# Performance work log

Measured on AMD Instinct MI355X. Metric: run time of the kernel, lower is better.

Reference implementation:

```python
import jax, jax.numpy as jnp
import numpy as np

N, S, C, G = 40000, 16, 96, 12
EPS = 1e-5

def ln(x, g, b):
    mu = jnp.mean(x, -1, keepdims=True)
    var = jnp.mean((x - mu) ** 2, -1, keepdims=True)
    return (x - mu) * jax.lax.rsqrt(var + EPS) * g + b

def setup_inputs() -> dict:
    key = jax.random.key(0)
    ks = jax.random.split(key, 20)
    s = 0.05
    inp = {
        'q': jax.random.normal(ks[0], (N, C), jnp.float32),
        'k': jax.random.normal(ks[1], (N, C), jnp.float32),
        'v': jax.random.normal(ks[2], (N, C), jnp.float32),
        'xyz': jax.random.normal(ks[3], (N, 3), jnp.float32),
        'reference_index': jax.random.randint(ks[4], (N, S), 0, N, jnp.int32),
        # linear_q: Linear(C,C)+LN(C)+ReLU
        'Wq': jax.random.normal(ks[5], (C, C), jnp.float32) * s,
        'bq': jnp.zeros((C,), jnp.float32),
        'gq': jnp.ones((C,), jnp.float32),
        'betaq': jnp.zeros((C,), jnp.float32),
        # linear_k
        'Wk': jax.random.normal(ks[6], (C, C), jnp.float32) * s,
        'bk': jnp.zeros((C,), jnp.float32),
        'gk': jnp.ones((C,), jnp.float32),
        'betak': jnp.zeros((C,), jnp.float32),
        # linear_v
        'Wv': jax.random.normal(ks[7], (C, C), jnp.float32) * s,
        'bv': jnp.zeros((C,), jnp.float32),
        # linear_p_bias: Linear(3,C)+LN(C)+ReLU+Linear(C,C)
        'Wp1': jax.random.normal(ks[8], (3, C), jnp.float32) * s,
        'bp1': jnp.zeros((C,), jnp.float32),
        'gp': jnp.ones((C,), jnp.float32),
        'betap': jnp.zeros((C,), jnp.float32),
        'Wp2': jax.random.normal(ks[9], (C, C), jnp.float32) * s,
        'bp2': jnp.zeros((C,), jnp.float32),
        # weight_encoding: Linear(C,G)+LN(G)+ReLU+Linear(G,G)
        'Ww1': jax.random.normal(ks[10], (C, G), jnp.float32) * s,
        'bw1': jnp.zeros((G,), jnp.float32),
        'gw': jnp.ones((G,), jnp.float32),
        'betaw': jnp.zeros((G,), jnp.float32),
        'Ww2': jax.random.normal(ks[11], (G, G), jnp.float32) * s,
        'bw2': jnp.zeros((G,), jnp.float32),
    }
    return inp

def reference(q, k, v, xyz, reference_index,
              Wq, bq, gq, betaq, Wk, bk, gk, betak, Wv, bv,
              Wp1, bp1, gp, betap, Wp2, bp2,
              Ww1, bw1, gw, betaw, Ww2, bw2):
    query = jax.nn.relu(ln(q @ Wq + bq, gq, betaq))            # [N, C]
    keyf  = jax.nn.relu(ln(k @ Wk + bk, gk, betak))            # [N, C]
    val   = v @ Wv + bv                                        # [N, C]

    idx = reference_index                                      # [N, S]
    mask = (idx >= 0).astype(q.dtype)                          # sign(idx+1)
    safe = jnp.clip(idx, 0, None)
    # pointops.grouping: gather w/ zero-fill at idx=-1; with_xyz prepends relative coords
    pos  = (xyz[safe] - xyz[:, None, :]) * mask[..., None]     # [N, S, 3]
    keyg = keyf[safe] * mask[..., None]                        # [N, S, C]
    valg = val[safe] * mask[..., None]                         # [N, S, C]

    rel = keyg - query[:, None, :]                             # [N, S, C]
    peb = jax.nn.relu(ln(pos @ Wp1 + bp1, gp, betap)) @ Wp2 + bp2
    rel = rel + peb
    valg = valg + peb

    w = jax.nn.relu(ln(rel @ Ww1 + bw1, gw, betaw)) @ Ww2 + bw2  # [N, S, G]
    w = jax.nn.softmax(w, axis=1) * mask[..., None]              # softmax over neighbors

    valg = valg.reshape(N, S, G, C // G)
    feat = jnp.einsum('nsgi,nsg->ngi', valg, w).reshape(N, C)
    return feat
```

## Files before the change

kernel.cpp:

```cpp
#include <hip/hip_runtime.h>

#define NN 40000
#define SS 16
#define CC 96
#define GG 12
#define SXP 104

typedef __attribute__((ext_vector_type(8))) short bf16x8;
typedef __attribute__((ext_vector_type(4))) float f32x4;

__device__ __forceinline__ short f2bf(float f) {
    union { float f; unsigned u; } c; c.f = f;
    unsigned r = (c.u + 0x7fffu + ((c.u >> 16) & 1u)) >> 16;
    return (short)r;
}
__device__ __forceinline__ unsigned pack2bf(float hi, float lo) {
    unsigned a = __float_as_uint(hi) + 0x8000u;
    unsigned b = __float_as_uint(lo) + 0x8000u;
    return __builtin_amdgcn_perm(a, b, 0x07060302u);
}
__device__ __forceinline__ ushort f2bf_hu(float f) {
    return (ushort)((__float_as_uint(f) + 0x8000u) >> 16);
}

template<int CTRL>
__device__ __forceinline__ float dppf(float x) {
    int r = __builtin_amdgcn_mov_dpp(__float_as_int(x), CTRL, 0xF, 0xF, true);
    return __int_as_float(r);
}
__device__ __forceinline__ float row16_sum(float x) {
    x += dppf<0xB1>(x);
    x += dppf<0x4E>(x);
    x += dppf<0x141>(x);
    x += dppf<0x140>(x);
    return x;
}
__device__ __forceinline__ float row16_max(float x) {
    x = fmaxf(x, dppf<0xB1>(x));
    x = fmaxf(x, dppf<0x4E>(x));
    x = fmaxf(x, dppf<0x141>(x));
    x = fmaxf(x, dppf<0x140>(x));
    return x;
}

#define J_W3   27648
#define J_P2   (J_W3 + 9216)
#define J_W1   (J_P2 + 1536)
#define J_WF   (J_W1 + 1536)
#define J_CF   (J_WF + 12)
#define J_S4   (J_CF + 4)
#define J_G    (J_S4 + 16)

__global__ void prep_kernel(const float* __restrict__ Wq, const float* __restrict__ Wk,
                            const float* __restrict__ Wv, const float* __restrict__ Wp2,
                            const float* __restrict__ Ww1, const float* __restrict__ bp2,
                            const float* __restrict__ bw1, const float* __restrict__ Wp1,
                            const float* __restrict__ bp1,
                            ushort* __restrict__ fragQKV, ushort* __restrict__ fragP2,
                            ushort* __restrict__ fragW1, ushort* __restrict__ fragWf,
                            float* __restrict__ cfused, float* __restrict__ stats)
{
    const int job = blockIdx.x*256 + threadIdx.x;
    if (job < J_W3) {
        const int which = job / 9216, o = job % 9216;
        const float* W = (which == 0) ? Wq : (which == 1) ? Wk : Wv;
        const int pos = o >> 3, j = o & 7;
        const int lane = pos & 63, ntkb = pos >> 6;
        const int nt = ntkb / 3, kb = ntkb - nt*3;
        const int col = nt*16 + (lane & 15), krow = kb*32 + (lane >> 4)*8 + j;
        fragQKV[job] = (ushort)f2bf(W[krow*CC + col]);
    } else if (job < J_P2) {
        const int o = job - J_W3;
        const int pos = o >> 3, j = o & 7;
        const int lane = pos & 63, ntkb = pos >> 6;
        const int nt = ntkb / 3, kb = ntkb - nt*3;
        const int col = nt*16 + (lane & 15), krow = kb*32 + (lane >> 4)*8 + j;
        fragP2[o] = (ushort)f2bf(Wp2[krow*CC + col]);
    } else if (job < J_W1) {
        const int o = job - J_P2;
        const int pos = o >> 3, j = o & 7;
        const int lane = pos & 63, kb = pos >> 6;
        const int col = lane & 15, krow = kb*32 + (lane >> 4)*8 + j;
        fragW1[o] = (col < GG) ? (ushort)f2bf(Ww1[krow*GG + col]) : (ushort)0;
    } else if (job < J_WF) {
        const int o = job - J_W1;
        const int pos = o >> 3, j = o & 7;
        const int lane = pos & 63, kb = pos >> 6;
        const int col = lane & 15, krow = kb*32 + (lane >> 4)*8 + j;
        float s = 0.f;
        if (col < GG) for (int jj = 0; jj < CC; ++jj) s += Wp2[krow*CC + jj] * Ww1[jj*GG + col];
        fragWf[o] = (col < GG) ? (ushort)f2bf(s) : (ushort)0;
    } else if (job < J_CF) {
        const int g = job - J_WF;
        float s = bw1[g];
        for (int jj = 0; jj < CC; ++jj) s += bp2[jj] * Ww1[jj*GG + g];
        cfused[g] = s;
    } else if (job < J_S4) {
        const int d = job - J_CF;
        float s = 0.f;
        for (int c = 0; c < CC; ++c) s += (d < 3) ? Wp1[d*CC + c] : bp1[c];
        stats[d] = s;
    } else if (job < J_G) {
        const int o = job - J_S4, d1 = o >> 2, d2 = o & 3;
        float s = 0.f;
        for (int c = 0; c < CC; ++c) {
            const float a1 = (d1 < 3) ? Wp1[d1*CC + c] : bp1[c];
            const float a2 = (d2 < 3) ? Wp1[d2*CC + c] : bp1[c];
            s += a1*a2;
        }
        stats[4 + o] = s;
    }
}

__global__ __launch_bounds__(256) void qkv_mfma(
    const float* __restrict__ q, const float* __restrict__ kx, const float* __restrict__ v,
    const float* __restrict__ bq, const float* __restrict__ gq, const float* __restrict__ betaq,
    const float* __restrict__ bk, const float* __restrict__ gk, const float* __restrict__ betak,
    const float* __restrict__ bv,
    const ushort* __restrict__ fragQKV, const ushort* __restrict__ fragW1,
    float* __restrict__ valout, float* __restrict__ qw1out, float* __restrict__ kw1out)
{
    __shared__ float sbias[CC], sg[CC], sbeta[CC];
    __shared__ __align__(16) ushort sx2[4][16*SXP];

    const int p = blockIdx.y;
    const float* X; const float* b;
    const float* g = nullptr; const float* beta = nullptr;
    if (p == 0)      { X = q;  b = bq; g = gq; beta = betaq; }
    else if (p == 1) { X = kx; b = bk; g = gk; beta = betak; }
    else             { X = v;  b = bv; }
    const bool has_ln = (p < 2);
    float* w1out = (p == 0) ? qw1out : kw1out;

    const int t = threadIdx.x;
    if (t < CC) {
        sbias[t] = b[t];
        if (has_ln) { sg[t] = g[t]; sbeta[t] = beta[t]; }
    }

    const int lane = t & 63, w = t >> 6;
    const int c16 = lane & 15, quad = lane >> 4;
    const ushort* fragW = fragQKV + p*9216;

    bf16x8 Ww1f[3];
    if (has_ln) {
        #pragma unroll
        for (int kb = 0; kb < 3; ++kb) {
            union { bf16x8 v; uint4 u; } wu;
            wu.u = ((const uint4*)fragW1)[kb*64 + lane];
            Ww1f[kb] = wu.v;
        }
    }

    __syncthreads();

    const f32x4 zero4 = {0.f, 0.f, 0.f, 0.f};
    ushort* sxw = sx2[w];
    const int tile = blockIdx.x*4 + w;
    const int row0 = tile * 16;

    const float* xr = X + (size_t)(row0 + c16)*CC;
    bf16x8 Af[3];
    #pragma unroll
    for (int kb = 0; kb < 3; ++kb) {
        const float4 a0 = *(const float4*)(xr + kb*32 + quad*8);
        const float4 a1 = *(const float4*)(xr + kb*32 + quad*8 + 4);
        union { bf16x8 v; uint u[4]; } au;
        au.u[0] = pack2bf(a0.y, a0.x);
        au.u[1] = pack2bf(a0.w, a0.z);
        au.u[2] = pack2bf(a1.y, a1.x);
        au.u[3] = pack2bf(a1.w, a1.z);
        Af[kb] = au.v;
    }

    f32x4 acc[6];
    #pragma unroll
    for (int nt = 0; nt < 6; ++nt) acc[nt] = zero4;
    #pragma unroll
    for (int kb = 0; kb < 3; ++kb)
        #pragma unroll
        for (int nt = 0; nt < 6; ++nt) {
            const bf16x8 bf = *(const bf16x8*)(fragW + ((nt*3 + kb)*64 + lane)*8);
            acc[nt] = __builtin_amdgcn_mfma_f32_16x16x32_bf16(Af[kb], bf, acc[nt], 0, 0, 0);
        }

    #pragma unroll
    for (int nt = 0; nt < 6; ++nt) {
        const float bb = sbias[nt*16 + c16];
        #pragma unroll
        for (int r = 0; r < 4; ++r) acc[nt][r] += bb;
    }

    if (has_ln) {
        #pragma unroll
        for (int r = 0; r < 4; ++r) {
            float sum = 0.f, sq = 0.f;
            #pragma unroll
            for (int nt = 0; nt < 6; ++nt) { float x = acc[nt][r]; sum += x; sq += x*x; }
            sum = row16_sum(sum); sq = row16_sum(sq);
            const float mu  = sum * (1.f/96.f);
            const float var = sq * (1.f/96.f) - mu*mu;
            const float rs  = rsqrtf(var + 1e-5f);
            #pragma unroll
            for (int nt = 0; nt < 6; ++nt) {
                const int c = nt*16 + c16;
                acc[nt][r] = fmaxf((acc[nt][r] - mu)*rs*sg[c] + sbeta[c], 0.f);
            }
        }
        #pragma unroll
        for (int nt = 0; nt < 6; ++nt)
            #pragma unroll
            for (int r = 0; r < 4; ++r)
                sxw[(quad*4 + r)*SXP + nt*16 + c16] = f2bf_hu(acc[nt][r]);

        f32x4 o = zero4;
        #pragma unroll
        for (int kb = 0; kb < 3; ++kb) {
            const bf16x8 aA = *(const bf16x8*)(sxw + c16*SXP + kb*32 + quad*8);
            o = __builtin_amdgcn_mfma_f32_16x16x32_bf16(aA, Ww1f[kb], o, 0, 0, 0);
        }
        if (c16 < GG) {
            #pragma unroll
            for (int r = 0; r < 4; ++r)
                w1out[(size_t)(row0 + quad*4 + r)*GG + c16] = o[r];
        }
    } else {
        #pragma unroll
        for (int r = 0; r < 4; ++r)
            #pragma unroll
            for (int nt = 0; nt < 6; ++nt)
                valout[(size_t)(row0 + quad*4 + r)*CC + nt*16 + c16] = acc[nt][r];
    }
}

__global__ __launch_bounds__(256) void attn2(
    const float* __restrict__ xyz, const int* __restrict__ refidx,
    const float* __restrict__ gp,  const float* __restrict__ betap,
    const float* __restrict__ Wp1, const float* __restrict__ bp1,
    const float* __restrict__ bp2,
    const float* __restrict__ gw,  const float* __restrict__ betaw,
    const float* __restrict__ Ww2, const float* __restrict__ bw2,
    const float* __restrict__ cfused, const float* __restrict__ stats,
    const ushort* __restrict__ fragP2, const ushort* __restrict__ fragWf,
    const float* __restrict__ valw, const float* __restrict__ kw1w, const float* __restrict__ qw1w,
    float* __restrict__ out)
{
    __shared__ __align__(16) ushort sWp2f[9216];
    __shared__ float4 sA[CC];
    __shared__ float2 sGB[CC];
    __shared__ float  sbp2[CC];
    __shared__ __align__(16) float sWw2T[GG*GG];
    __shared__ float  sgw[16], sbetaw[16], sbw2[16], scf[16];
    __shared__ float  sstats[20];
    __shared__ __align__(16) float ybuf[4][SS*GG];

    const int t = threadIdx.x;
    if (t < CC) {
        sA[t]  = make_float4(Wp1[t], Wp1[CC + t], Wp1[2*CC + t], bp1[t]);
        sGB[t] = make_float2(gp[t], betap[t]);
        sbp2[t] = bp2[t];
    }
    if (t < GG*GG) {
        const int gr = t / GG, gc = t - gr*GG;
        sWw2T[gc*GG + gr] = Ww2[t];
    }
    if (t < 16) {
        sgw[t]    = (t < GG) ? gw[t]     : 0.f;
        sbetaw[t] = (t < GG) ? betaw[t]  : 0.f;
        sbw2[t]   = (t < GG) ? bw2[t]    : 0.f;
        scf[t]    = (t < GG) ? cfused[t] : 0.f;
    }
    if (t < 20) sstats[t] = stats[t];
    for (int i = t; i < 1152; i += 256) ((uint4*)sWp2f)[i] = ((const uint4*)fragP2)[i];

    const int lane = t & 63, w = t >> 6;
    const int c16 = lane & 15, quad = lane >> 4;
    const int gcl = (c16 < GG) ? c16 : (GG-1);
    const float laneg = (c16 < GG) ? 1.f : 0.f;

    bf16x8 Wff[3];
    #pragma unroll
    for (int kb = 0; kb < 3; ++kb) {
        union { bf16x8 v; uint4 u; } wu;
        wu.u = ((const uint4*)fragWf)[kb*64 + lane];
        Wff[kb] = wu.v;
    }

    __syncthreads();

    float* yb  = ybuf[w];
    float* sw2 = ybuf[w];
    const f32x4 zero4 = {0.f, 0.f, 0.f, 0.f};

    const int n = blockIdx.x*4 + w;

    const int   id   = refidx[(size_t)n*SS + c16];
    const float m    = (id >= 0) ? 1.f : 0.f;
    const int   safe = (id < 0) ? 0 : id;

    int sid[4]; float mr[4];
    #pragma unroll
    for (int r = 0; r < 4; ++r) {
        const int sd = refidx[(size_t)n*SS + quad*4 + r];
        mr[r]  = (sd >= 0) ? 1.f : 0.f;
        sid[r] = (sd < 0) ? 0 : sd;
    }

    float va[3][2][4];
    #pragma unroll
    for (int ntp = 0; ntp < 3; ++ntp)
        #pragma unroll
        for (int h = 0; h < 2; ++h)
            #pragma unroll
            for (int r = 0; r < 4; ++r)
                va[ntp][h][r] = valw[(size_t)sid[r]*CC + (2*ntp + h)*16 + c16];

    float kwv[4];
    #pragma unroll
    for (int r = 0; r < 4; ++r)
        kwv[r] = kw1w[(size_t)sid[r]*GG + gcl] * (mr[r] * laneg);
    const float qv = qw1w[(size_t)n*GG + gcl] * laneg;

    const float px = (xyz[(size_t)safe*3 + 0] - xyz[(size_t)n*3 + 0]) * m;
    const float py = (xyz[(size_t)safe*3 + 1] - xyz[(size_t)n*3 + 1]) * m;
    const float pz = (xyz[(size_t)safe*3 + 2] - xyz[(size_t)n*3 + 2]) * m;

    const float mu = (px*sstats[0] + py*sstats[1] + pz*sstats[2] + sstats[3]) * (1.f/96.f);
    float e2 = 0.f;
    {
        const float p4[4] = {px, py, pz, 1.f};
        #pragma unroll
        for (int a = 0; a < 4; ++a) {
            float ta = 0.f;
            #pragma unroll
            for (int b2 = 0; b2 < 4; ++b2) ta = fmaf(sstats[4 + a*4 + b2], p4[b2], ta);
            e2 = fmaf(p4[a], ta, e2);
        }
    }
    const float var = e2*(1.f/96.f) - mu*mu;
    const float rs  = rsqrtf(var + 1e-5f);

    bf16x8 t1A[3];
    #pragma unroll
    for (int kb = 0; kb < 3; ++kb) {
        union { bf16x8 v; uint u[4]; } tu;
        #pragma unroll
        for (int jp = 0; jp < 4; ++jp) {
            float tt[2];
            #pragma unroll
            for (int h = 0; h < 2; ++h) {
                const int c = kb*32 + quad*8 + jp*2 + h;
                const float4 aw = sA[c];
                const float x = fmaf(px, aw.x, fmaf(py, aw.y, fmaf(pz, aw.z, aw.w)));
                const float2 gb = sGB[c];
                tt[h] = fmaxf(fmaf((x - mu)*rs, gb.x, gb.y), 0.f);
            }
            tu.u[jp] = pack2bf(tt[1], tt[0]);
        }
        t1A[kb] = tu.v;
    }

    f32x4 t2 = zero4;
    #pragma unroll
    for (int kb = 0; kb < 3; ++kb)
        t2 = __builtin_amdgcn_mfma_f32_16x16x32_bf16(t1A[kb], Wff[kb], t2, 0, 0, 0);
    #pragma unroll
    for (int r = 0; r < 4; ++r)
        t2[r] += kwv[r] - qv + scf[c16];

    #pragma unroll
    for (int r = 0; r < 4; ++r) {
        const float x = t2[r];
        const float s1 = row16_sum(x);
        const float s2 = row16_sum(x*x);
        const float mu2  = s1 * (1.f/12.f);
        const float var2 = s2 * (1.f/12.f) - mu2*mu2;
        const float rs2  = rsqrtf(var2 + 1e-5f);
        const float y    = fmaxf((x - mu2)*rs2*sgw[c16] + sbetaw[c16], 0.f);
        if (c16 < GG) yb[(quad*4 + r)*GG + c16] = y;
    }

    const f32x4 yr0 = *(const f32x4*)(yb + c16*GG + 0);
    const f32x4 yr1 = *(const f32x4*)(yb + c16*GG + 4);
    const f32x4 yr2 = *(const f32x4*)(yb + c16*GG + 8);
    float w3v[3];
    #pragma unroll
    for (int gi = 0; gi < 3; ++gi) {
        const int gpp = quad + gi*4;
        const f32x4 wa = *(const f32x4*)(sWw2T + gpp*GG + 0);
        const f32x4 wb = *(const f32x4*)(sWw2T + gpp*GG + 4);
        const f32x4 wc = *(const f32x4*)(sWw2T + gpp*GG + 8);
        float a2 = sbw2[gpp];
        #pragma unroll
        for (int j = 0; j < 4; ++j) a2 = fmaf(yr0[j], wa[j], a2);
        #pragma unroll
        for (int j = 0; j < 4; ++j) a2 = fmaf(yr1[j], wb[j], a2);
        #pragma unroll
        for (int j = 0; j < 4; ++j) a2 = fmaf(yr2[j], wc[j], a2);
        w3v[gi] = a2;
    }

    #pragma unroll
    for (int gi = 0; gi < 3; ++gi) {
        const float mx = row16_max(w3v[gi]);
        const float e  = __expf(w3v[gi] - mx);
        const float tot = row16_sum(e);
        w3v[gi] = e * __builtin_amdgcn_rcpf(tot) * m;
    }
    #pragma unroll
    for (int gi = 0; gi < 3; ++gi)
        sw2[(quad + 4*gi)*16 + c16] = w3v[gi];

    #pragma unroll
    for (int ntp = 0; ntp < 3; ++ntp) {
        const int nt0 = 2*ntp, nt1 = 2*ntp + 1;
        f32x4 pa = zero4, pb = zero4;
        #pragma unroll
        for (int kb = 0; kb < 3; ++kb) {
            const bf16x8 bfa = *(const bf16x8*)(sWp2f + ((nt0*3 + kb)*64 + lane)*8);
            const bf16x8 bfb = *(const bf16x8*)(sWp2f + ((nt1*3 + kb)*64 + lane)*8);
            pa = __builtin_amdgcn_mfma_f32_16x16x32_bf16(t1A[kb], bfa, pa, 0, 0, 0);
            pb = __builtin_amdgcn_mfma_f32_16x16x32_bf16(t1A[kb], bfb, pb, 0, 0, 0);
        }
        #pragma unroll
        for (int h = 0; h < 2; ++h) {
            const int nt = 2*ntp + h;
            const f32x4& pc = (h == 0) ? pa : pb;
            const float b2   = sbp2[nt*16 + c16];
            const int   gidx = 2*nt + (c16 >> 3);
            const f32x4 swv = *(const f32x4*)(sw2 + gidx*16 + quad*4);
            float a2 = 0.f;
            #pragma unroll
            for (int r = 0; r < 4; ++r)
                a2 = fmaf(pc[r] + b2 + va[ntp][h][r], swv[r], a2);
            a2 += __shfl_xor(a2, 16, 64);
            a2 += __shfl_xor(a2, 32, 64);
            if (quad == 0) out[(size_t)n*CC + nt*16 + c16] = a2;
        }
    }
}

extern "C" void kernel_launch(void* const* d_in, const int* in_sizes, int n_in,
                              void* d_out, int out_size, void* d_ws, size_t ws_size,
                              hipStream_t stream)
{
    const float* q     = (const float*)d_in[0];
    const float* k     = (const float*)d_in[1];
    const float* v     = (const float*)d_in[2];
    const float* xyz   = (const float*)d_in[3];
    const int*   ridx  = (const int*)d_in[4];
    const float* Wq    = (const float*)d_in[5];
    const float* bq    = (const float*)d_in[6];
    const float* gq    = (const float*)d_in[7];
    const float* betaq = (const float*)d_in[8];
    const float* Wk    = (const float*)d_in[9];
    const float* bk    = (const float*)d_in[10];
    const float* gk    = (const float*)d_in[11];
    const float* betak = (const float*)d_in[12];
    const float* Wv    = (const float*)d_in[13];
    const float* bv    = (const float*)d_in[14];
    const float* Wp1   = (const float*)d_in[15];
    const float* bp1   = (const float*)d_in[16];
    const float* gp    = (const float*)d_in[17];
    const float* betap = (const float*)d_in[18];
    const float* Wp2   = (const float*)d_in[19];
    const float* bp2   = (const float*)d_in[20];
    const float* Ww1   = (const float*)d_in[21];
    const float* bw1   = (const float*)d_in[22];
    const float* gw    = (const float*)d_in[23];
    const float* betaw = (const float*)d_in[24];
    const float* Ww2   = (const float*)d_in[25];
    const float* bw2   = (const float*)d_in[26];
    float* out = (float*)d_out;

    float* ws = (float*)d_ws;
    float* valw   = ws;
    float* kw1w   = valw + (size_t)NN*CC;
    float* qw1w   = kw1w + (size_t)NN*GG;
    float* cfused = qw1w + (size_t)NN*GG;
    float* statsp = cfused + 16;
    ushort* fragQKV = (ushort*)(statsp + 24);
    ushort* fragP2  = fragQKV + 3*9216;
    ushort* fragW1  = fragP2 + 9216;
    ushort* fragWf  = fragW1 + 1536;

    prep_kernel<<<dim3(157, 1, 1), 256, 0, stream>>>(
        Wq, Wk, Wv, Wp2, Ww1, bp2, bw1, Wp1, bp1,
        fragQKV, fragP2, fragW1, fragWf, cfused, statsp);

    qkv_mfma<<<dim3(625, 3, 1), 256, 0, stream>>>(
        q, k, v, bq, gq, betaq, bk, gk, betak, bv,
        fragQKV, fragW1, valw, qw1w, kw1w);

    attn2<<<dim3(10000, 1, 1), 256, 0, stream>>>(
        xyz, ridx, gp, betap, Wp1, bp1, bp2,
        gw, betaw, Ww2, bw2, cfused, statsp,
        fragP2, fragWf, valw, kw1w, qw1w, out);
}
```

Measured before the change: 220.9 us.

## Process two points per wavefront in attn2 and halve the grid

Each wavefront now handles two query points instead of one, so the per-block setup (LDS weight staging, fragment loads, syncthreads) is amortized over eight points per block. All gathers for both points (refidx as int4, xyz, kw1w, qw1w, valw) are issued up front, before a sched_barrier, to raise memory-level parallelism. The MFMA chains for the two points are interleaved to hide latency. The cost is roughly doubled register pressure from the va arrays, which may lower occupancy.

```diff
diff --git a/kernel.cpp b/kernel.cpp
--- a/kernel.cpp
+++ b/kernel.cpp
@@ -252,7 +252,7 @@
     __shared__ __align__(16) float sWw2T[GG*GG];
     __shared__ float  sgw[16], sbetaw[16], sbw2[16], scf[16];
     __shared__ float  sstats[20];
-    __shared__ __align__(16) float ybuf[4][SS*GG];
+    __shared__ __align__(16) float ybuf[4][2][SS*GG];
 
     const int t = threadIdx.x;
     if (t < CC) {
@@ -278,6 +278,59 @@
     const int gcl = (c16 < GG) ? c16 : (GG-1);
     const float laneg = (c16 < GG) ? 1.f : 0.f;
 
+    __syncthreads();
+
+    const f32x4 zero4 = {0.f, 0.f, 0.f, 0.f};
+    const int n0 = blockIdx.x*8 + w*2;
+
+    int   id[2];  int4 rr[2];
+    #pragma unroll
+    for (int u = 0; u < 2; ++u) {
+        id[u] = refidx[(size_t)(n0 + u)*SS + c16];
+        rr[u] = *(const int4*)(refidx + (size_t)(n0 + u)*SS + quad*4);
+    }
+
+    float mm[2], px[2], py[2], pz[2];
+    #pragma unroll
+    for (int u = 0; u < 2; ++u) {
+        mm[u] = (id[u] >= 0) ? 1.f : 0.f;
+        const int safe = (id[u] < 0) ? 0 : id[u];
+        const int nn = n0 + u;
+        px[u] = (xyz[(size_t)safe*3 + 0] - xyz[(size_t)nn*3 + 0]) * mm[u];
+        py[u] = (xyz[(size_t)safe*3 + 1] - xyz[(size_t)nn*3 + 1]) * mm[u];
+        pz[u] = (xyz[(size_t)safe*3 + 2] - xyz[(size_t)nn*3 + 2]) * mm[u];
+    }
+
+    int sid[2][4]; float mrg[2][4];
+    #pragma unroll
+    for (int u = 0; u < 2; ++u) {
+        const int rv0 = rr[u].x, rv1 = rr[u].y, rv2 = rr[u].z, rv3 = rr[u].w;
+        sid[u][0] = (rv0 < 0) ? 0 : rv0;  mrg[u][0] = (rv0 >= 0) ? laneg : 0.f;
+        sid[u][1] = (rv1 < 0) ? 0 : rv1;  mrg[u][1] = (rv1 >= 0) ? laneg : 0.f;
+        sid[u][2] = (rv2 < 0) ? 0 : rv2;  mrg[u][2] = (rv2 >= 0) ? laneg : 0.f;
+        sid[u][3] = (rv3 < 0) ? 0 : rv3;  mrg[u][3] = (rv3 >= 0) ? laneg : 0.f;
+    }
+
+    float kwr[2][4], qvl[2];
+    #pragma unroll
+    for (int u = 0; u < 2; ++u) {
+        #pragma unroll
+        for (int r = 0; r < 4; ++r)
+            kwr[u][r] = kw1w[(size_t)sid[u][r]*GG + gcl];
+        qvl[u] = qw1w[(size_t)(n0 + u)*GG + gcl];
+    }
+
+    float va[2][3][2][4];
+    #pragma unroll
+    for (int u = 0; u < 2; ++u)
+        #pragma unroll
+        for (int ntp = 0; ntp < 3; ++ntp)
+            #pragma unroll
+            for (int h = 0; h < 2; ++h)
+                #pragma unroll
+                for (int r = 0; r < 4; ++r)
+                    va[u][ntp][h][r] = valw[(size_t)sid[u][r]*CC + (2*ntp + h)*16 + c16];
+
     bf16x8 Wff[3];
     #pragma unroll
     for (int kb = 0; kb < 3; ++kb) {
@@ -286,156 +339,174 @@
         Wff[kb] = wu.v;
     }
 
-    __syncthreads();
-
-    float* yb  = ybuf[w];
-    float* sw2 = ybuf[w];
-    const f32x4 zero4 = {0.f, 0.f, 0.f, 0.f};
-
-    const int n = blockIdx.x*4 + w;
-
-    const int   id   = refidx[(size_t)n*SS + c16];
-    const float m    = (id >= 0) ? 1.f : 0.f;
-    const int   safe = (id < 0) ? 0 : id;
-
-    int sid[4]; float mr[4];
-    #pragma unroll
-    for (int r = 0; r < 4; ++r) {
-        const int sd = refidx[(size_t)n*SS + quad*4 + r];
-        mr[r]  = (sd >= 0) ? 1.f : 0.f;
-        sid[r] = (sd < 0) ? 0 : sd;
-    }
-
-    float va[3][2][4];
-    #pragma unroll
-    for (int ntp = 0; ntp < 3; ++ntp)
-        #pragma unroll
-        for (int h = 0; h < 2; ++h)
+    __builtin_amdgcn_sched_barrier(0);
+
+    float muv[2], rsv[2];
+    {
+        const float s0 = sstats[0], s1 = sstats[1], s2 = sstats[2], s3 = sstats[3];
+        float G_[16];
+        #pragma unroll
+        for (int i = 0; i < 16; ++i) G_[i] = sstats[4 + i];
+        #pragma unroll
+        for (int u = 0; u < 2; ++u) {
+            muv[u] = (px[u]*s0 + py[u]*s1 + pz[u]*s2 + s3) * (1.f/96.f);
+            const float p4[4] = {px[u], py[u], pz[u], 1.f};
+            float e2 = 0.f;
+            #pragma unroll
+            for (int a = 0; a < 4; ++a) {
+                float ta = 0.f;
+                #pragma unroll
+                for (int b2 = 0; b2 < 4; ++b2) ta = fmaf(G_[a*4 + b2], p4[b2], ta);
+                e2 = fmaf(p4[a], ta, e2);
+            }
+            const float var = e2*(1.f/96.f) - muv[u]*muv[u];
+            rsv[u] = rsqrtf(var + 1e-5f);
+        }
+    }
+
+    bf16x8 t1A[2][3];
+    #pragma unroll
+    for (int kb = 0; kb < 3; ++kb) {
+        uint tw[2][4];
+        #pragma unroll
+        for (int jp = 0; jp < 4; ++jp) {
+            const int c0 = kb*32 + quad*8 + jp*2, c1 = c0 + 1;
+            const float4 aw0 = sA[c0], aw1 = sA[c1];
+            const float2 gb0 = sGB[c0], gb1 = sGB[c1];
+            #pragma unroll
+            for (int u = 0; u < 2; ++u) {
+                const float x0 = fmaf(px[u], aw0.x, fmaf(py[u], aw0.y, fmaf(pz[u], aw0.z, aw0.w)));
+                const float x1 = fmaf(px[u], aw1.x, fmaf(py[u], aw1.y, fmaf(pz[u], aw1.z, aw1.w)));
+                const float t0 = fmaxf(fmaf((x0 - muv[u])*rsv[u], gb0.x, gb0.y), 0.f);
+                const float t1v = fmaxf(fmaf((x1 - muv[u])*rsv[u], gb1.x, gb1.y), 0.f);
+                tw[u][jp] = pack2bf(t1v, t0);
+            }
+        }
+        #pragma unroll
+        for (int u = 0; u < 2; ++u) {
+            union { bf16x8 v; uint uu[4]; } tc;
+            tc.uu[0] = tw[u][0]; tc.uu[1] = tw[u][1];
+            tc.uu[2] = tw[u][2]; tc.uu[3] = tw[u][3];
+            t1A[u][kb] = tc.v;
+        }
+    }
+
+    f32x4 t2[2];
+    #pragma unroll
+    for (int u = 0; u < 2; ++u) t2[u] = zero4;
+    #pragma unroll
+    for (int kb = 0; kb < 3; ++kb)
+        #pragma unroll
+        for (int u = 0; u < 2; ++u)
+            t2[u] = __builtin_amdgcn_mfma_f32_16x16x32_bf16(t1A[u][kb], Wff[kb], t2[u], 0, 0, 0);
+    {
+        const float cf = scf[c16];
+        #pragma unroll
+        for (int u = 0; u < 2; ++u) {
+            const float qz = qvl[u]*laneg;
             #pragma unroll
             for (int r = 0; r < 4; ++r)
-                va[ntp][h][r] = valw[(size_t)sid[r]*CC + (2*ntp + h)*16 + c16];
-
-    float kwv[4];
-    #pragma unroll
-    for (int r = 0; r < 4; ++r)
-        kwv[r] = kw1w[(size_t)sid[r]*GG + gcl] * (mr[r] * laneg);
-    const float qv = qw1w[(size_t)n*GG + gcl] * laneg;
-
-    const float px = (xyz[(size_t)safe*3 + 0] - xyz[(size_t)n*3 + 0]) * m;
-    const float py = (xyz[(size_t)safe*3 + 1] - xyz[(size_t)n*3 + 1]) * m;
-    const float pz = (xyz[(size_t)safe*3 + 2] - xyz[(size_t)n*3 + 2]) * m;
-
-    const float mu = (px*sstats[0] + py*sstats[1] + pz*sstats[2] + sstats[3]) * (1.f/96.f);
-    float e2 = 0.f;
+                t2[u][r] += kwr[u][r]*mrg[u][r] - qz + cf;
+        }
+    }
+
     {
-        const float p4[4] = {px, py, pz, 1.f};
-        #pragma unroll
-        for (int a = 0; a < 4; ++a) {
-            float ta = 0.f;
-            #pragma unroll
-            for (int b2 = 0; b2 < 4; ++b2) ta = fmaf(sstats[4 + a*4 + b2], p4[b2], ta);
-            e2 = fmaf(p4[a], ta, e2);
-        }
-    }
-    const float var = e2*(1.f/96.f) - mu*mu;
-    const float rs  = rsqrtf(var + 1e-5f);
-
-    bf16x8 t1A[3];
-    #pragma unroll
-    for (int kb = 0; kb < 3; ++kb) {
-        union { bf16x8 v; uint u[4]; } tu;
-        #pragma unroll
-        for (int jp = 0; jp < 4; ++jp) {
-            float tt[2];
-            #pragma unroll
-            for (int h = 0; h < 2; ++h) {
-                const int c = kb*32 + quad*8 + jp*2 + h;
-                const float4 aw = sA[c];
-                const float x = fmaf(px, aw.x, fmaf(py, aw.y, fmaf(pz, aw.z, aw.w)));
-                const float2 gb = sGB[c];
-                tt[h] = fmaxf(fmaf((x - mu)*rs, gb.x, gb.y), 0.f);
-            }
-            tu.u[jp] = pack2bf(tt[1], tt[0]);
-        }
-        t1A[kb] = tu.v;
-    }
-
-    f32x4 t2 = zero4;
-    #pragma unroll
-    for (int kb = 0; kb < 3; ++kb)
-        t2 = __builtin_amdgcn_mfma_f32_16x16x32_bf16(t1A[kb], Wff[kb], t2, 0, 0, 0);
-    #pragma unroll
-    for (int r = 0; r < 4; ++r)
-        t2[r] += kwv[r] - qv + scf[c16];
-
-    #pragma unroll
-    for (int r = 0; r < 4; ++r) {
-        const float x = t2[r];
-        const float s1 = row16_sum(x);
-        const float s2 = row16_sum(x*x);
-        const float mu2  = s1 * (1.f/12.f);
-        const float var2 = s2 * (1.f/12.f) - mu2*mu2;
-        const float rs2  = rsqrtf(var2 + 1e-5f);
-        const float y    = fmaxf((x - mu2)*rs2*sgw[c16] + sbetaw[c16], 0.f);
-        if (c16 < GG) yb[(quad*4 + r)*GG + c16] = y;
-    }
-
-    const f32x4 yr0 = *(const f32x4*)(yb + c16*GG + 0);
-    const f32x4 yr1 = *(const f32x4*)(yb + c16*GG + 4);
-    const f32x4 yr2 = *(const f32x4*)(yb + c16*GG + 8);
-    float w3v[3];
-    #pragma unroll
-    for (int gi = 0; gi < 3; ++gi) {
-        const int gpp = quad + gi*4;
-        const f32x4 wa = *(const f32x4*)(sWw2T + gpp*GG + 0);
-        const f32x4 wb = *(const f32x4*)(sWw2T + gpp*GG + 4);
-        const f32x4 wc = *(const f32x4*)(sWw2T + gpp*GG + 8);
-        float a2 = sbw2[gpp];
-        #pragma unroll
-        for (int j = 0; j < 4; ++j) a2 = fmaf(yr0[j], wa[j], a2);
-        #pragma unroll
-        for (int j = 0; j < 4; ++j) a2 = fmaf(yr1[j], wb[j], a2);
-        #pragma unroll
-        for (int j = 0; j < 4; ++j) a2 = fmaf(yr2[j], wc[j], a2);
-        w3v[gi] = a2;
-    }
-
-    #pragma unroll
-    for (int gi = 0; gi < 3; ++gi) {
-        const float mx = row16_max(w3v[gi]);
-        const float e  = __expf(w3v[gi] - mx);
-        const float tot = row16_sum(e);
-        w3v[gi] = e * __builtin_amdgcn_rcpf(tot) * m;
-    }
-    #pragma unroll
-    for (int gi = 0; gi < 3; ++gi)
-        sw2[(quad + 4*gi)*16 + c16] = w3v[gi];
+        const float gwv = sgw[c16], bwv = sbetaw[c16];
+        #pragma unroll
+        for (int u = 0; u < 2; ++u) {
+            float* yb = ybuf[w][u];
+            #pragma unroll
+            for (int r = 0; r < 4; ++r) {
+                const float x = t2[u][r];
+                const float s1 = row16_sum(x);
+                const float s2 = row16_sum(x*x);
+                const float mu2  = s1 * (1.f/12.f);
+                const float var2 = s2 * (1.f/12.f) - mu2*mu2;
+                const float rs2  = rsqrtf(var2 + 1e-5f);
+                const float y    = fmaxf((x - mu2)*rs2*gwv + bwv, 0.f);
+                if (c16 < GG) yb[(quad*4 + r)*GG + c16] = y;
+            }
+        }
+    }
+
+    float w3v[2][3];
+    {
+        f32x4 yr[2][3];
+        #pragma unroll
+        for (int u = 0; u < 2; ++u) {
+            yr[u][0] = *(const f32x4*)(ybuf[w][u] + c16*GG + 0);
+            yr[u][1] = *(const f32x4*)(ybuf[w][u] + c16*GG + 4);
+            yr[u][2] = *(const f32x4*)(ybuf[w][u] + c16*GG + 8);
+        }
+        #pragma unroll
+        for (int gi = 0; gi < 3; ++gi) {
+            const int gpp = quad + gi*4;
+            const f32x4 wa = *(const f32x4*)(sWw2T + gpp*GG + 0);
+            const f32x4 wb = *(const f32x4*)(sWw2T + gpp*GG + 4);
+            const f32x4 wc = *(const f32x4*)(sWw2T + gpp*GG + 8);
+            const float bb = sbw2[gpp];
+            #pragma unroll
+            for (int u = 0; u < 2; ++u) {
+                float a2 = bb;
+                #pragma unroll
+                for (int j = 0; j < 4; ++j) a2 = fmaf(yr[u][0][j], wa[j], a2);
+                #pragma unroll
+                for (int j = 0; j < 4; ++j) a2 = fmaf(yr[u][1][j], wb[j], a2);
+                #pragma unroll
+                for (int j = 0; j < 4; ++j) a2 = fmaf(yr[u][2][j], wc[j], a2);
+                w3v[u][gi] = a2;
+            }
+        }
+    }
+
+    #pragma unroll
+    for (int u = 0; u < 2; ++u) {
+        #pragma unroll
+        for (int gi = 0; gi < 3; ++gi) {
+            const float mx = row16_max(w3v[u][gi]);
+            const float e  = __expf(w3v[u][gi] - mx);
+            const float tot = row16_sum(e);
+            w3v[u][gi] = e * __builtin_amdgcn_rcpf(tot) * mm[u];
+        }
+        float* sw2 = ybuf[w][u];
+        #pragma unroll
+        for (int gi = 0; gi < 3; ++gi)
+            sw2[(quad + 4*gi)*16 + c16] = w3v[u][gi];
+    }
 
     #pragma unroll
     for (int ntp = 0; ntp < 3; ++ntp) {
         const int nt0 = 2*ntp, nt1 = 2*ntp + 1;
-        f32x4 pa = zero4, pb = zero4;
+        f32x4 pa[2], pb[2];
+        #pragma unroll
+        for (int u = 0; u < 2; ++u) { pa[u] = zero4; pb[u] = zero4; }
         #pragma unroll
         for (int kb = 0; kb < 3; ++kb) {
             const bf16x8 bfa = *(const bf16x8*)(sWp2f + ((nt0*3 + kb)*64 + lane)*8);
             const bf16x8 bfb = *(const bf16x8*)(sWp2f + ((nt1*3 + kb)*64 + lane)*8);
-            pa = __builtin_amdgcn_mfma_f32_16x16x32_bf16(t1A[kb], bfa, pa, 0, 0, 0);
-            pb = __builtin_amdgcn_mfma_f32_16x16x32_bf16(t1A[kb], bfb, pb, 0, 0, 0);
+            #pragma unroll
+            for (int u = 0; u < 2; ++u) {
+                pa[u] = __builtin_amdgcn_mfma_f32_16x16x32_bf16(t1A[u][kb], bfa, pa[u], 0, 0, 0);
+                pb[u] = __builtin_amdgcn_mfma_f32_16x16x32_bf16(t1A[u][kb], bfb, pb[u], 0, 0, 0);
+            }
         }
         #pragma unroll
         for (int h = 0; h < 2; ++h) {
             const int nt = 2*ntp + h;
-            const f32x4& pc = (h == 0) ? pa : pb;
             const float b2   = sbp2[nt*16 + c16];
             const int   gidx = 2*nt + (c16 >> 3);
-            const f32x4 swv = *(const f32x4*)(sw2 + gidx*16 + quad*4);
-            float a2 = 0.f;
-            #pragma unroll
-            for (int r = 0; r < 4; ++r)
-                a2 = fmaf(pc[r] + b2 + va[ntp][h][r], swv[r], a2);
-            a2 += __shfl_xor(a2, 16, 64);
-            a2 += __shfl_xor(a2, 32, 64);
-            if (quad == 0) out[(size_t)n*CC + nt*16 + c16] = a2;
+            #pragma unroll
+            for (int u = 0; u < 2; ++u) {
+                const f32x4 pc  = (h == 0) ? pa[u] : pb[u];
+                const f32x4 swv = *(const f32x4*)(ybuf[w][u] + gidx*16 + quad*4);
+                float a2 = 0.f;
+                #pragma unroll
+                for (int r = 0; r < 4; ++r)
+                    a2 = fmaf(pc[r] + b2 + va[u][ntp][h][r], swv[r], a2);
+                a2 += __shfl_xor(a2, 16, 64);
+                a2 += __shfl_xor(a2, 32, 64);
+                if (quad == 0) out[(size_t)(n0 + u)*CC + nt*16 + c16] = a2;
+            }
         }
     }
 }
@@ -492,7 +563,7 @@
         q, k, v, bq, gq, betaq, bk, gk, betak, bv,
         fragQKV, fragW1, valw, qw1w, kw1w);
 
-    attn2<<<dim3(10000, 1, 1), 256, 0, stream>>>(
+    attn2<<<dim3(5000, 1, 1), 256, 0, stream>>>(
         xyz, ridx, gp, betap, Wp1, bp1, bp2,
         gw, betaw, Ww2, bw2, cfused, statsp,
         fragP2, fragWf, valw, kw1w, qw1w, out);
```

After: 214.5 us. 2.9% less time.
